# Kernel optimization log

Measured on AMD Instinct MI355X. Metric: run time of the kernel, lower is better.

The kernel has to match this reference:

```python
import jax, jax.numpy as jnp
import numpy as np

_DN = ('NCHW', 'OIHW', 'NCHW')


def setup_inputs() -> dict:
    key = jax.random.key(0)
    k1, k2 = jax.random.split(key)
    x = jax.random.normal(k1, (32, 3, 224, 224), dtype=jnp.float32)
    memes = jax.random.normal(k2, (64, 3, 7, 7), dtype=jnp.float32)
    return {"x": x, "memes": memes}


def reference(x, memes):
    # x: [B, C, H, W], memes: [K, C, kh, kw]
    # x_m = cross-correlation of x with templates -> [B, K, H', W']
    x_m = jax.lax.conv_general_dilated(x, memes, window_strides=(1, 1),
                                       padding='VALID', dimension_numbers=_DN)
    # x2 = conv2d(x**2, ones_like(memes)): every output channel is identical
    # (all-ones kernel), so compute once with a single-channel ones kernel and
    # let broadcasting replicate it across the K template channels.
    ones_k = jnp.ones((1,) + memes.shape[1:], dtype=x.dtype)  # [1, C, kh, kw]
    x2 = jax.lax.conv_general_dilated(x * x, ones_k, window_strides=(1, 1),
                                      padding='VALID', dimension_numbers=_DN)  # [B,1,H',W']
    # m2 = sum(weight**2 over (2,3), keepdim).sum(dim=1) -> [K, 1, 1]
    m2 = jnp.sum(memes * memes, axis=(1, 2, 3)).reshape(-1, 1, 1)
    # Normalized squared Euclidean distance between each patch and template.
    return (x2 - 2.0 * x_m + m2) / m2
```

## Files before the change

### kernel.cpp

```cpp
#include <hip/hip_runtime.h>

#define NB 32
#define NC 3
#define NK 64
#define KS 7
#define IH 224
#define IW 224
#define OH 218
#define OW 218
#define OHW (OH * OW)
#define ROWS 8

typedef float  f32x4  __attribute__((ext_vector_type(4)));
typedef float  f32x16 __attribute__((ext_vector_type(16)));
typedef short  s16x8  __attribute__((ext_vector_type(8)));
typedef unsigned long long u64;

static __device__ __forceinline__ unsigned short f2bf(float f) {
  unsigned int u = __float_as_uint(f);
  u += 0x7FFFu + ((u >> 16) & 1u);
  return (unsigned short)(u >> 16);
}

static __device__ __forceinline__ int swz2(int t, int ci) {
  return ((((ci >> 3) + (t >> 2)) & 3) << 3) | (ci & 7);
}


__global__ void k_prep_xrow(const float* __restrict__ x, unsigned short* __restrict__ xb,
                            float* __restrict__ t) {
  __shared__ float s_lds[IW];
  const int n  = blockIdx.x;
  const int b  = n / IH;
  const int h  = n - b * IH;
  const int px = threadIdx.x;
  if (px < IW) {
    float acc = 0.f;
#pragma unroll
    for (int c = 0; c < NC; ++c) {
      size_t idx = ((size_t)(b * NC + c) * IH + h) * IW + px;
      float v = x[idx];
      xb[idx] = f2bf(v);
      acc += v * v;
    }
    s_lds[px] = acc;
  }
  __syncthreads();
  if (px < OW) {
    float acc = 0.f;
#pragma unroll
    for (int j = 0; j < KS; ++j) acc += s_lds[px + j];
    t[(size_t)(b * IH + h) * OW + px] = acc;
  }
}

__global__ void k_prep_w(const float* __restrict__ memes, unsigned short* __restrict__ WTg,
                         float* __restrict__ m2inv) {
  __shared__ float red[3];
  const int k = blockIdx.x, t = threadIdx.x;
  float v = 0.f;
  if (t < 147) v = memes[k * 147 + t];
  float s = v * v;
#pragma unroll
  for (int sh = 32; sh > 0; sh >>= 1) s += __shfl_down(s, sh, 64);
  if ((t & 63) == 0) red[t >> 6] = s;
  __syncthreads();
  if (t == 0) m2inv[k] = 1.0f / (red[0] + red[1] + red[2]);
  if (t < 147) {
    int c = t / 49, rem = t - 49 * c, i = rem / 7, j = rem - 7 * i;
    WTg[(j * NK + k) * 32 + (c * 7 + i)] = f2bf(v);
  }
  for (int idx = t; idx < 7 * 11; idx += 192) {
    int j = idx / 11, ci = 21 + (idx - 11 * j);
    WTg[(j * NK + k) * 32 + ci] = 0;
  }
}

static __device__ __forceinline__ void xt_issue(u64 v[2],
    const unsigned short* __restrict__ xb, int b, int oh, int ow0, int tid) {
#pragma unroll
  for (int m = 0; m < 2; ++m) {
    int idx = tid + 256 * m;
    u64 val = 0;
    if (idx < 378) {
      int tq = idx % 18;
      int ci = idx / 18;
      int c  = ci / 7;
      int i  = ci - 7 * c;
      val = *(const u64*)&xb[((size_t)(b * NC + c) * IH + oh + i) * IW + ow0 + 4 * tq];
    }
    v[m] = val;
  }
}

static __device__ __forceinline__ void xt_write(unsigned short* __restrict__ XT,
    const u64 v[2], int tid) {
#pragma unroll
  for (int m = 0; m < 2; ++m) {
    int idx = tid + 256 * m;
    if (idx < 378) {
      int tq = idx % 18;
      int ci = idx / 18;
#pragma unroll
      for (int e = 0; e < 4; ++e) {
        int t = 4 * tq + e;
        XT[t * 32 + swz2(t, ci)] = (unsigned short)(v[m] >> (16 * e));
      }
    }
  }
}

__global__ __launch_bounds__(256, 3) void k_main(
    const unsigned short* __restrict__ xb, const float* __restrict__ tg,
    const unsigned short* __restrict__ WTg, const float* __restrict__ m2inv,
    float* __restrict__ out) {
  __shared__ __align__(16) unsigned short XTl[2][72 * 32];

  const int tid  = threadIdx.x;
  const int w    = tid >> 6;
  const int lane = tid & 63;
  const int l31  = lane & 31;
  const int hsel = lane >> 5;
  const int kh   = w >> 1;
  const int ph   = w & 1;

  const int wg  = blockIdx.x;
  const int sw  = (wg & 7) * 448 + (wg >> 3);
  const int ow0 = (sw & 3) * 64;
  const int ohb = ((sw >> 2) % 28) * ROWS;
  const int b   = sw / 112;

  s16x8 Af0[KS], Af1[KS];
  {
    const unsigned short* ap = WTg + (size_t)(kh * 32 + l31) * 32 + hsel * 8;
#pragma unroll
    for (int j = 0; j < KS; ++j) {
      Af0[j] = *(const s16x8*)&ap[(size_t)j * (NK * 32)];
      Af1[j] = *(const s16x8*)&ap[(size_t)j * (NK * 32) + 16];
    }
  }

  f32x4 m2r[4];
  {
    const float* mp = m2inv + kh * 32 + 4 * hsel;
#pragma unroll
    for (int g = 0; g < 4; ++g) m2r[g] = *(const f32x4*)&mp[8 * g];
  }

  for (int idx = tid; idx < 2 * 72; idx += 256) {
    int bb = idx / 72, t = idx - 72 * bb;
    unsigned short* row = &XTl[bb][t * 32];
    const int m = (t >> 2) & 3;
    *(uint4*)&row[((3 + m) & 3) << 3] = (uint4){0, 0, 0, 0};
    const int b2 = ((2 + m) & 3) << 3;
    row[b2 + 5] = 0; row[b2 + 6] = 0; row[b2 + 7] = 0;
  }

  u64 s0[2];
  xt_issue(s0, xb, b, ohb, ow0, tid);
  xt_write(&XTl[0][0], s0, tid);
  asm volatile("s_waitcnt lgkmcnt(0)" ::: "memory");
  __builtin_amdgcn_s_barrier();

  const int tB = ph * 32 + l31;
  const int ow = ow0 + tB;

#pragma unroll 1
  for (int r = 0; r < ROWS; ++r) {
    const int oh = ohb + r;
    const bool more = (r + 1 < ROWS);

    u64 sn[2];
    if (more) xt_issue(sn, xb, b, oh + 1, ow0, tid);

    const bool ok = (ow < OW) && (oh < OH);

    float x2v = 0.f;
    if (ok) {
      const float* tp = tg + ((size_t)b * IH + oh) * OW + ow;
#pragma unroll
      for (int i = 0; i < KS; ++i) x2v += tp[i * OW];
    }

    const unsigned short* XT = &XTl[r & 1][0];
    f32x16 accA = {0.f,0.f,0.f,0.f,0.f,0.f,0.f,0.f,0.f,0.f,0.f,0.f,0.f,0.f,0.f,0.f};
    f32x16 accB = accA;

#pragma unroll
    for (int j = 0; j < KS; ++j) {
      const int t = tB + j;
      const unsigned short* br = XT + t * 32;
      const int m = (t >> 2) & 3;
      s16x8 bA = *(const s16x8*)&br[((hsel + m) & 3) << 3];
      s16x8 bB = *(const s16x8*)&br[((2 + hsel + m) & 3) << 3];
      accA = __builtin_amdgcn_mfma_f32_32x32x16_bf16(Af0[j], bA, accA, 0, 0, 0);
      accB = __builtin_amdgcn_mfma_f32_32x32x16_bf16(Af1[j], bB, accB, 0, 0, 0);
    }
    const f32x16 acc = accA + accB;

    if (ok) {
      float* ob = out + ((size_t)(b * NK + kh * 32) * OH + oh) * OW + ow;
#pragma unroll
      for (int reg = 0; reg < 16; ++reg) {
        const int kk = (reg & 3) + 8 * (reg >> 2) + 4 * hsel;
        ob[(size_t)kk * OHW] = (x2v - 2.0f * acc[reg]) * m2r[reg >> 2][reg & 3] + 1.0f;
      }
    }

    if (more) {
      xt_write(&XTl[(r + 1) & 1][0], sn, tid);
      asm volatile("s_waitcnt lgkmcnt(0)" ::: "memory");
      __builtin_amdgcn_s_barrier();
    }
  }
}

extern "C" void kernel_launch(void* const* d_in, const int* in_sizes, int n_in,
                              void* d_out, int out_size, void* d_ws, size_t ws_size,
                              hipStream_t stream) {
  const float* x     = (const float*)d_in[0];
  const float* memes = (const float*)d_in[1];
  float* out = (float*)d_out;

  char* ws = (char*)d_ws;
  unsigned short* xb  = (unsigned short*)(ws);
  float* t            = (float*)(ws + 9633792);
  unsigned short* WTg = (unsigned short*)(ws + 15884288);
  float* m2inv        = (float*)(ws + 15912960);

  (void)in_sizes; (void)n_in; (void)out_size; (void)ws_size;

  k_prep_xrow<<<NB * IH, 256, 0, stream>>>(x, xb, t);
  k_prep_w<<<NK, 192, 0, stream>>>(memes, WTg, m2inv);

  k_main<<<4 * 28 * NB, 256, 0, stream>>>(xb, t, WTg, m2inv, out);
}
```

Before: 151.0 us.

## Give each wave a private LDS input tile to remove block barriers

Each wave now stages its own 40-column slice of the bf16 input rows into a private double-buffered LDS region, where before all four waves filled one 72-column tile shared across the workgroup. This removes the workgroup-wide s_barrier and lgkmcnt wait after every row, so waves run independently. In exchange, each wave issues more global loads, since the two waves sharing a column half load the same data, and LDS use grows. Correctness now depends on lockstep execution within a wave, with no explicit wave-level fence between the LDS writes and the later reads.

```diff
diff --git a/kernel.cpp b/kernel.cpp
--- a/kernel.cpp
+++ b/kernel.cpp
@@ -76,34 +76,34 @@
   }
 }
 
-static __device__ __forceinline__ void xt_issue(u64 v[2],
-    const unsigned short* __restrict__ xb, int b, int oh, int ow0, int tid) {
-#pragma unroll
-  for (int m = 0; m < 2; ++m) {
-    int idx = tid + 256 * m;
+static __device__ __forceinline__ void xtw_issue(u64 v[4],
+    const unsigned short* __restrict__ xb, int b, int oh, int owb, int lane) {
+#pragma unroll
+  for (int m = 0; m < 4; ++m) {
+    int idx = lane + 64 * m;
     u64 val = 0;
-    if (idx < 378) {
-      int tq = idx % 18;
-      int ci = idx / 18;
+    if (idx < 210) {
+      int ci = idx / 10;
+      int q  = idx - 10 * ci;
       int c  = ci / 7;
       int i  = ci - 7 * c;
-      val = *(const u64*)&xb[((size_t)(b * NC + c) * IH + oh + i) * IW + ow0 + 4 * tq];
+      val = *(const u64*)&xb[((size_t)(b * NC + c) * IH + oh + i) * IW + owb + 4 * q];
     }
     v[m] = val;
   }
 }
 
-static __device__ __forceinline__ void xt_write(unsigned short* __restrict__ XT,
-    const u64 v[2], int tid) {
-#pragma unroll
-  for (int m = 0; m < 2; ++m) {
-    int idx = tid + 256 * m;
-    if (idx < 378) {
-      int tq = idx % 18;
-      int ci = idx / 18;
+static __device__ __forceinline__ void xtw_write(unsigned short* __restrict__ XT,
+    const u64 v[4], int lane) {
+#pragma unroll
+  for (int m = 0; m < 4; ++m) {
+    int idx = lane + 64 * m;
+    if (idx < 210) {
+      int ci = idx / 10;
+      int q  = idx - 10 * ci;
 #pragma unroll
       for (int e = 0; e < 4; ++e) {
-        int t = 4 * tq + e;
+        int t = 4 * q + e;
         XT[t * 32 + swz2(t, ci)] = (unsigned short)(v[m] >> (16 * e));
       }
     }
@@ -114,7 +114,7 @@
     const unsigned short* __restrict__ xb, const float* __restrict__ tg,
     const unsigned short* __restrict__ WTg, const float* __restrict__ m2inv,
     float* __restrict__ out) {
-  __shared__ __align__(16) unsigned short XTl[2][72 * 32];
+  __shared__ __align__(16) unsigned short XTw[4][2][40 * 32];
 
   const int tid  = threadIdx.x;
   const int w    = tid >> 6;
@@ -130,6 +130,8 @@
   const int ohb = ((sw >> 2) % 28) * ROWS;
   const int b   = sw / 112;
 
+  const int owb = ow0 + ph * 32;
+
   s16x8 Af0[KS], Af1[KS];
   {
     const unsigned short* ap = WTg + (size_t)(kh * 32 + l31) * 32 + hsel * 8;
@@ -147,31 +149,30 @@
     for (int g = 0; g < 4; ++g) m2r[g] = *(const f32x4*)&mp[8 * g];
   }
 
-  for (int idx = tid; idx < 2 * 72; idx += 256) {
-    int bb = idx / 72, t = idx - 72 * bb;
-    unsigned short* row = &XTl[bb][t * 32];
+  unsigned short* myXT[2] = {&XTw[w][0][0], &XTw[w][1][0]};
+
+  for (int idx = lane; idx < 2 * 40; idx += 64) {
+    int bb = idx / 40, t = idx - 40 * bb;
+    unsigned short* row = myXT[bb] + t * 32;
     const int m = (t >> 2) & 3;
     *(uint4*)&row[((3 + m) & 3) << 3] = (uint4){0, 0, 0, 0};
     const int b2 = ((2 + m) & 3) << 3;
     row[b2 + 5] = 0; row[b2 + 6] = 0; row[b2 + 7] = 0;
   }
 
-  u64 s0[2];
-  xt_issue(s0, xb, b, ohb, ow0, tid);
-  xt_write(&XTl[0][0], s0, tid);
-  asm volatile("s_waitcnt lgkmcnt(0)" ::: "memory");
-  __builtin_amdgcn_s_barrier();
-
-  const int tB = ph * 32 + l31;
-  const int ow = ow0 + tB;
+  u64 s0[4];
+  xtw_issue(s0, xb, b, ohb, owb, lane);
+  xtw_write(myXT[0], s0, lane);
+
+  const int ow = owb + l31;
 
 #pragma unroll 1
   for (int r = 0; r < ROWS; ++r) {
     const int oh = ohb + r;
     const bool more = (r + 1 < ROWS);
 
-    u64 sn[2];
-    if (more) xt_issue(sn, xb, b, oh + 1, ow0, tid);
+    u64 sn[4];
+    if (more) xtw_issue(sn, xb, b, oh + 1, owb, lane);
 
     const bool ok = (ow < OW) && (oh < OH);
 
@@ -182,13 +183,13 @@
       for (int i = 0; i < KS; ++i) x2v += tp[i * OW];
     }
 
-    const unsigned short* XT = &XTl[r & 1][0];
+    const unsigned short* XT = myXT[r & 1];
     f32x16 accA = {0.f,0.f,0.f,0.f,0.f,0.f,0.f,0.f,0.f,0.f,0.f,0.f,0.f,0.f,0.f,0.f};
     f32x16 accB = accA;
 
 #pragma unroll
     for (int j = 0; j < KS; ++j) {
-      const int t = tB + j;
+      const int t = l31 + j;
       const unsigned short* br = XT + t * 32;
       const int m = (t >> 2) & 3;
       s16x8 bA = *(const s16x8*)&br[((hsel + m) & 3) << 3];
@@ -207,11 +208,7 @@
       }
     }
 
-    if (more) {
-      xt_write(&XTl[(r + 1) & 1][0], sn, tid);
-      asm volatile("s_waitcnt lgkmcnt(0)" ::: "memory");
-      __builtin_amdgcn_s_barrier();
-    }
+    if (more) xtw_write(myXT[(r + 1) & 1], sn, lane);
   }
 }
 
```

New measurement: 314.5 us. 108% more time.
